# Kernel tuning notes

Measured on AMD Instinct MI355X. Metric: run time of the kernel, lower is better.

The kernel has to match this reference:

```python
import jax, jax.numpy as jnp
import numpy as np
import math

def _ln(x, g, b, eps=1e-5):
    mu = x.mean(-1, keepdims=True)
    var = ((x - mu) ** 2).mean(-1, keepdims=True)
    return (x - mu) / jnp.sqrt(var + eps) * g + b

def _mha(x, in_w, in_b, out_w, out_b, nh):
    # torch nn.MultiheadAttention (batch_first, eval): q,k,v chunks of in_proj
    Bn, Nn, Dm = x.shape
    hd = Dm // nh
    q, k, v = jnp.split(x @ in_w.T + in_b, 3, axis=-1)
    sp = lambda t: t.reshape(Bn, Nn, nh, hd).transpose(0, 2, 1, 3)
    q, k, v = sp(q), sp(k), sp(v)
    a = jax.nn.softmax(jnp.einsum('bhid,bhjd->bhij', q, k) / math.sqrt(hd), axis=-1)
    y = jnp.einsum('bhij,bhjd->bhid', a, v).transpose(0, 2, 1, 3).reshape(Bn, Nn, Dm)
    return y @ out_w.T + out_b

def setup_inputs():
    key = jax.random.key(0)
    ks = iter(jax.random.split(key, 40))
    nrm = lambda shape: jax.random.normal(next(ks), shape, jnp.float32) * 0.02
    B, T, C, H, W = 2, 32, 3, 64, 64
    D, P, nL, nS = 512, 8, 6, 3
    N = (H // P) ** 2
    z = lambda *s: jnp.zeros(s, jnp.float32)
    o = lambda *s: jnp.ones(s, jnp.float32)
    return dict(
        x=jax.random.normal(next(ks), (B, T, C, H, W), jnp.float32),
        patch_w=nrm((D, C * P * P)), patch_b=z(D),
        tok_ln_g=o(D), tok_ln_b=z(D),
        spatial_pos=nrm((1, 1, N, D)), temporal_pos=nrm((1, T, 1, D)),
        snorm_g=o(D), snorm_b=z(D),
        sa_in_w=nrm((nS, 3 * D, D)), sa_in_b=z(nS, 3 * D),
        sa_out_w=nrm((nS, D, D)), sa_out_b=z(nS, D),
        ln1_g=o(nL, D), ln1_b=z(nL, D),
        kqv_w=nrm((nL, 3 * D, D)), kqv_b=z(nL, 3 * D),
        proj_w=nrm((nL, D, D)), proj_b=z(nL, D),
        ln2_g=o(nL, D), ln2_b=z(nL, D),
        fc_w=nrm((nL, 4 * D, D)), fc_b=z(nL, 4 * D),
        cproj_w=nrm((nL, D, 4 * D)), cproj_b=z(nL, D),
        lnf_g=o(D), lnf_b=z(D),
        th_w1=nrm((D // 2, D)), th_b1=z(D // 2), th_w2=nrm((1, D // 2)), th_b2=z(1),
        sh_w1=nrm((D // 2, D)), sh_b1=z(D // 2), sh_w2=nrm((1, D // 2)), sh_b2=z(1),
        pf_w1=nrm((D // 2, D)), pf_b1=z(D // 2), pf_w2=nrm((1, D // 2)), pf_b2=z(1),
    )

def reference(x, patch_w, patch_b, tok_ln_g, tok_ln_b, spatial_pos, temporal_pos,
              snorm_g, snorm_b, sa_in_w, sa_in_b, sa_out_w, sa_out_b,
              ln1_g, ln1_b, kqv_w, kqv_b, proj_w, proj_b, ln2_g, ln2_b,
              fc_w, fc_b, cproj_w, cproj_b, lnf_g, lnf_b,
              th_w1, th_b1, th_w2, th_b2, sh_w1, sh_b1, sh_w2, sh_b2,
              pf_w1, pf_b1, pf_w2, pf_b2):
    B, T, C, H, W = x.shape
    D = patch_w.shape[0]
    P = int(math.isqrt(patch_w.shape[1] // C))
    Hn, Wn = H // P, W // P
    N = Hn * Wn
    # Conv3d kernel=(1,P,P), stride=(1,P,P) == per-frame patchify + matmul
    patches = x.reshape(B, T, C, Hn, P, Wn, P).transpose(0, 1, 3, 5, 2, 4, 6).reshape(B, T, N, C * P * P)
    tok = _ln(patches @ patch_w.T + patch_b, tok_ln_g, tok_ln_b)
    tok = tok + spatial_pos + temporal_pos[:, :T]
    # per-frame spatial attention: identical math per frame -> batch over B*T
    s = tok.reshape(B * T, N, D)
    for i in range(sa_in_w.shape[0]):
        s = s + _mha(_ln(s, snorm_g, snorm_b), sa_in_w[i], sa_in_b[i], sa_out_w[i], sa_out_b[i], nh=4)
    L = T * N
    hid = s.reshape(B, L, D)
    nh = 8
    hd = D // nh
    mask = jnp.tril(jnp.ones((L, L), bool))  # causal over T*N tokens
    for i in range(kqv_w.shape[0]):
        a_in = _ln(hid, ln1_g[i], ln1_b[i])
        k, q, v = jnp.split(a_in @ kqv_w[i].T + kqv_b[i], 3, axis=-1)  # torch split order: k, q, v
        sp = lambda t: t.reshape(B, L, nh, hd).transpose(0, 2, 1, 3)
        q, k, v = sp(q), sp(k), sp(v)
        att = jnp.einsum('bhid,bhjd->bhij', q, k) / math.sqrt(hd)
        att = jax.nn.softmax(jnp.where(mask, att, -jnp.inf), axis=-1)
        y = jnp.einsum('bhij,bhjd->bhid', att, v).transpose(0, 2, 1, 3).reshape(B, L, D)
        hid = hid + y @ proj_w[i].T + proj_b[i]
        m_in = _ln(hid, ln2_g[i], ln2_b[i])
        h = jax.nn.gelu(m_in @ fc_w[i].T + fc_b[i], approximate=False)
        hid = hid + h @ cproj_w[i].T + cproj_b[i]
    hid = _ln(hid, lnf_g, lnf_b).reshape(B, T, N, D)
    head = lambda zz, w1, b1, w2, b2: jax.nn.leaky_relu(zz @ w1.T + b1, 0.2) @ w2.T + b2
    tf = hid.mean(axis=2)  # [B, T, D]
    temporal_score = head(tf[:, -1], th_w1, th_b1, th_w2, th_b2)  # [B, 1] (last timestep, full lengths)
    spatial_score = head(hid.mean(axis=1).mean(axis=1), sh_w1, sh_b1, sh_w2, sh_b2)
    per_frame_scores = head(tf, pf_w1, pf_b1, pf_w2, pf_b2)  # [B, T, 1]
    final_score = temporal_score + spatial_score + per_frame_scores.mean(axis=1)
    return (temporal_score, spatial_score, per_frame_scores, final_score)
```

## Files before the change

### kernel.cpp

```cpp
#include <hip/hip_runtime.h>
#include <hip/hip_bf16.h>
#include <math.h>

#define MTOK 4096

typedef __bf16 bf16x8 __attribute__((ext_vector_type(8)));
typedef float f32x4 __attribute__((ext_vector_type(4)));

__device__ __forceinline__ ushort f2bf(float f){
  __hip_bfloat16 h = __float2bfloat16(f);
  return *reinterpret_cast<ushort*>(&h);
}
__device__ __forceinline__ float bf2f(ushort u){
  return __uint_as_float(((uint)u) << 16);
}
__device__ __forceinline__ void gload_lds16(const void* g, void* l){
  __builtin_amdgcn_global_load_lds((__attribute__((address_space(1))) void*)(void*)g,
                                   (__attribute__((address_space(3))) void*)l, 16, 0, 0);
}

__device__ __forceinline__ float blockReduceSum(float v, float* red){
  #pragma unroll
  for (int off = 32; off; off >>= 1) v += __shfl_down(v, off, 64);
  int lane = threadIdx.x & 63, wid = threadIdx.x >> 6;
  __syncthreads();
  if (lane == 0) red[wid] = v;
  __syncthreads();
  float r = 0.f;
  int nw = blockDim.x >> 6;
  for (int i = 0; i < nw; i++) r += red[i];
  return r;
}
__device__ __forceinline__ float rowMax16(float v){
  #pragma unroll
  for (int m = 8; m; m >>= 1) v = fmaxf(v, __shfl_xor(v, m, 64));
  return v;
}
__device__ __forceinline__ float rowSum16(float v){
  #pragma unroll
  for (int m = 8; m; m >>= 1) v += __shfl_xor(v, m, 64);
  return v;
}

__global__ __launch_bounds__(256) void cvt_w_kernel(
    const float* __restrict__ src, ushort* __restrict__ dst, int n)
{
  int i = (blockIdx.x * 256 + threadIdx.x) * 8;
  float4 a = *(const float4*)(src + i);
  float4 b = *(const float4*)(src + i + 4);
  uint4 o;
  o.x = (uint)f2bf(a.x) | ((uint)f2bf(a.y) << 16);
  o.y = (uint)f2bf(a.z) | ((uint)f2bf(a.w) << 16);
  o.z = (uint)f2bf(b.x) | ((uint)f2bf(b.y) << 16);
  o.w = (uint)f2bf(b.z) | ((uint)f2bf(b.w) << 16);
  *(uint4*)(dst + i) = o;
}

#define OFF_PATCH 0u
#define OFF_SAIN  98304u
#define OFF_SAOUT 2457600u
#define OFF_KQV   3244032u
#define OFF_PROJ  7962624u
#define OFF_FC    9535488u
#define OFF_CPROJ 15826944u
#define W_TOTAL   22118400u
__global__ __launch_bounds__(256) void cvt_all_kernel(
    const float* __restrict__ pw, const float* __restrict__ sain,
    const float* __restrict__ saout, const float* __restrict__ kqv,
    const float* __restrict__ proj, const float* __restrict__ fc,
    const float* __restrict__ cproj, ushort* __restrict__ dst)
{
  int blk = blockIdx.x;
  const float* src; size_t off;
  if      (blk <    48){ src = pw;    off = OFF_PATCH; }
  else if (blk <  1200){ src = sain;  off = OFF_SAIN;  blk -= 48;   }
  else if (blk <  1584){ src = saout; off = OFF_SAOUT; blk -= 1200; }
  else if (blk <  3888){ src = kqv;   off = OFF_KQV;   blk -= 1584; }
  else if (blk <  4656){ src = proj;  off = OFF_PROJ;  blk -= 3888; }
  else if (blk <  7728){ src = fc;    off = OFF_FC;    blk -= 4656; }
  else                 { src = cproj; off = OFF_CPROJ; blk -= 7728; }
  size_t si = (size_t)blk*2048 + threadIdx.x*8;
  float4 a = *(const float4*)(src + si);
  float4 b = *(const float4*)(src + si + 4);
  uint4 o;
  o.x = (uint)f2bf(a.x) | ((uint)f2bf(a.y) << 16);
  o.y = (uint)f2bf(a.z) | ((uint)f2bf(a.w) << 16);
  o.z = (uint)f2bf(b.x) | ((uint)f2bf(b.y) << 16);
  o.w = (uint)f2bf(b.z) | ((uint)f2bf(b.w) << 16);
  *(uint4*)(dst + off + si) = o;
}

__global__ __launch_bounds__(256) void im2col_kernel(
    const float* __restrict__ x, ushort* __restrict__ Pm)
{
  int idx = blockIdx.x*256 + threadIdx.x;
  int m = idx / 24, e8 = idx % 24;
  int b = m >> 11, t = (m >> 6) & 31, n = m & 63;
  int hn = n >> 3, wn = n & 7;
  int c = e8 >> 3, ph = e8 & 7;
  const float* src = x + (((size_t)(b*32 + t)*3 + c)*64 + hn*8 + ph)*64 + wn*8;
  float4 a = *(const float4*)src;
  float4 bq = *(const float4*)(src + 4);
  uint4 o;
  o.x = (uint)f2bf(a.x) | ((uint)f2bf(a.y) << 16);
  o.y = (uint)f2bf(a.z) | ((uint)f2bf(a.w) << 16);
  o.z = (uint)f2bf(bq.x) | ((uint)f2bf(bq.y) << 16);
  o.w = (uint)f2bf(bq.z) | ((uint)f2bf(bq.w) << 16);
  *(uint4*)(Pm + (size_t)m*192 + e8*8) = o;
}

__global__ __launch_bounds__(256) void ln_pos_kernel(
    const float* __restrict__ in, float* __restrict__ out,
    const float* __restrict__ g, const float* __restrict__ b,
    const float* __restrict__ spos, const float* __restrict__ tpos)
{
  int r = blockIdx.x*4 + (threadIdx.x >> 6);
  int lane = threadIdx.x & 63;
  int n = r & 63, t = (r >> 6) & 31;
  const float* row = in + (size_t)r*512 + lane*8;
  float4 v0 = *(const float4*)row;
  float4 v1 = *(const float4*)(row + 4);
  float s = v0.x+v0.y+v0.z+v0.w+v1.x+v1.y+v1.z+v1.w;
  float q = v0.x*v0.x+v0.y*v0.y+v0.z*v0.z+v0.w*v0.w+v1.x*v1.x+v1.y*v1.y+v1.z*v1.z+v1.w*v1.w;
  #pragma unroll
  for (int m = 1; m < 64; m <<= 1){ s += __shfl_xor(s, m, 64); q += __shfl_xor(q, m, 64); }
  float mu = s*(1.f/512.f);
  float inv = rsqrtf(q*(1.f/512.f) - mu*mu + 1e-5f);
  const float* gp = g + lane*8;
  const float* bp = b + lane*8;
  const float* sp = spos + n*512 + lane*8;
  const float* tp = tpos + t*512 + lane*8;
  float* op = out + (size_t)r*512 + lane*8;
  #pragma unroll
  for (int e = 0; e < 2; e++){
    float4 vv = e ? v1 : v0;
    float4 gg = *(const float4*)(gp + e*4);
    float4 bb = *(const float4*)(bp + e*4);
    float4 ss = *(const float4*)(sp + e*4);
    float4 tt = *(const float4*)(tp + e*4);
    float4 oo;
    oo.x = (vv.x-mu)*inv*gg.x + bb.x + ss.x + tt.x;
    oo.y = (vv.y-mu)*inv*gg.y + bb.y + ss.y + tt.y;
    oo.z = (vv.z-mu)*inv*gg.z + bb.z + ss.z + tt.z;
    oo.w = (vv.w-mu)*inv*gg.w + bb.w + ss.w + tt.w;
    *(float4*)(op + e*4) = oo;
  }
}

__global__ __launch_bounds__(256) void ln_bf16_kernel(
    const float* __restrict__ in, ushort* __restrict__ out,
    const float* __restrict__ g, const float* __restrict__ b)
{
  int r = blockIdx.x*4 + (threadIdx.x >> 6);
  int lane = threadIdx.x & 63;
  const float* row = in + (size_t)r*512 + lane*8;
  float4 v0 = *(const float4*)row;
  float4 v1 = *(const float4*)(row + 4);
  float s = v0.x+v0.y+v0.z+v0.w+v1.x+v1.y+v1.z+v1.w;
  float q = v0.x*v0.x+v0.y*v0.y+v0.z*v0.z+v0.w*v0.w+v1.x*v1.x+v1.y*v1.y+v1.z*v1.z+v1.w*v1.w;
  #pragma unroll
  for (int m = 1; m < 64; m <<= 1){ s += __shfl_xor(s, m, 64); q += __shfl_xor(q, m, 64); }
  float mu = s*(1.f/512.f);
  float inv = rsqrtf(q*(1.f/512.f) - mu*mu + 1e-5f);
  float4 g0 = *(const float4*)(g + lane*8);
  float4 g1 = *(const float4*)(g + lane*8 + 4);
  float4 b0 = *(const float4*)(b + lane*8);
  float4 b1 = *(const float4*)(b + lane*8 + 4);
  uint4 o;
  o.x = (uint)f2bf((v0.x-mu)*inv*g0.x + b0.x) | ((uint)f2bf((v0.y-mu)*inv*g0.y + b0.y) << 16);
  o.y = (uint)f2bf((v0.z-mu)*inv*g0.z + b0.z) | ((uint)f2bf((v0.w-mu)*inv*g0.w + b0.w) << 16);
  o.z = (uint)f2bf((v1.x-mu)*inv*g1.x + b1.x) | ((uint)f2bf((v1.y-mu)*inv*g1.y + b1.y) << 16);
  o.w = (uint)f2bf((v1.z-mu)*inv*g1.z + b1.z) | ((uint)f2bf((v1.w-mu)*inv*g1.w + b1.w) << 16);
  *(uint4*)(out + (size_t)r*512 + lane*8) = o;
}

template<int BM, int BN, bool GELU, bool BF16OUT>
__global__ __launch_bounds__(256) void gemm2_kernel(
    const ushort* __restrict__ X, const ushort* __restrict__ Wb,
    const float* __restrict__ bias, const float* __restrict__ res,
    void* __restrict__ Yv, int M, int Nn, int K)
{
  constexpr int WROWS = (BN == 128) ? 2 : 4;
  constexpr int WM = BM / WROWS;
  constexpr int FM = WM / 16;
  constexpr int FN = 4;
  __shared__ __attribute__((aligned(16))) char smem[2*(BM+BN)*128];
  char* Xs0 = smem;
  char* Ws0 = smem + BM*128;
  char* Xs1 = smem + (BM+BN)*128;
  char* Ws1 = Xs1 + BM*128;
  int tid = threadIdx.x, lane = tid & 63, wv = tid >> 6;
  int bm = blockIdx.y * BM, bn = blockIdx.x * BN;
  int wm, wn;
  if (BN == 128){ wm = (wv >> 1) * WM; wn = (wv & 1) * 64; }
  else          { wm = wv * WM;        wn = 0; }

  f32x4 acc[FM][FN];
  #pragma unroll
  for (int i = 0; i < FM; i++)
    #pragma unroll
    for (int j = 0; j < FN; j++){ f32x4 z = {0.f,0.f,0.f,0.f}; acc[i][j] = z; }

  int rowoff = wv*8 + (lane >> 3);
  int colsrc = ((lane & 7) ^ (lane >> 3)) * 16;

  auto stage = [&](char* Xd, char* Wd, int k0){
    #pragma unroll
    for (int i = 0; i < BM/32; i++){
      int row = i*32 + rowoff;
      gload_lds16((const char*)(X + (size_t)(bm + row)*K + k0) + colsrc,
                  Xd + (i*32 + wv*8)*128);
    }
    #pragma unroll
    for (int i = 0; i < BN/32; i++){
      int row = i*32 + rowoff;
      gload_lds16((const char*)(Wb + (size_t)(bn + row)*K + k0) + colsrc,
                  Wd + (i*32 + wv*8)*128);
    }
  };

  stage(Xs0, Ws0, 0);
  __syncthreads();
  int nt = K >> 6;
  for (int t = 0; t < nt; t++){
    char* Xc = (t & 1) ? Xs1 : Xs0;
    char* Wc = (t & 1) ? Ws1 : Ws0;
    if (t + 1 < nt) stage((t & 1) ? Xs0 : Xs1, (t & 1) ? Ws0 : Ws1, (t+1)*64);
    #pragma unroll
    for (int kc = 0; kc < 2; kc++){
      bf16x8 a[FM], b[FN];
      #pragma unroll
      for (int f = 0; f < FM; f++){
        int ra = wm + f*16 + (lane & 15);
        a[f] = *(const bf16x8*)(Xc + ra*128 + ((kc*64 + (lane>>4)*16) ^ ((ra & 7) << 4)));
      }
      #pragma unroll
      for (int f = 0; f < FN; f++){
        int rb = wn + f*16 + (lane & 15);
        b[f] = *(const bf16x8*)(Wc + rb*128 + ((kc*64 + (lane>>4)*16) ^ ((rb & 7) << 4)));
      }
      #pragma unroll
      for (int i = 0; i < FM; i++)
        #pragma unroll
        for (int j = 0; j < FN; j++)
          acc[i][j] = __builtin_amdgcn_mfma_f32_16x16x32_bf16(a[i], b[j], acc[i][j], 0, 0, 0);
    }
    __syncthreads();
  }
  int col0 = lane & 15;
  float bv[FN];
  #pragma unroll
  for (int fn = 0; fn < FN; fn++) bv[fn] = bias[bn + wn + fn*16 + col0];
  #pragma unroll
  for (int fm = 0; fm < FM; fm++){
    #pragma unroll
    for (int r = 0; r < 4; r++){
      int m = bm + wm + fm*16 + (lane >> 4)*4 + r;
      #pragma unroll
      for (int fn = 0; fn < FN; fn++){
        int n = bn + wn + fn*16 + col0;
        float v = acc[fm][fn][r] + bv[fn];
        if (res) v += res[(size_t)m*Nn + n];
        if (GELU) v = 0.5f * v * (1.f + erff(v * 0.70710678118654752440f));
        if (BF16OUT) ((ushort*)Yv)[(size_t)m*Nn + n] = f2bf(v);
        else         ((float*) Yv)[(size_t)m*Nn + n] = v;
      }
    }
  }
}

__global__ __launch_bounds__(256) void spatial_attn_mfma_kernel(
    const ushort* __restrict__ qkv, ushort* __restrict__ y)
{
  __shared__ __attribute__((aligned(16))) char Ks[64*256];
  __shared__ __attribute__((aligned(16))) char Vt[128*128];
  __shared__ __attribute__((aligned(16))) char Ps[64*128];
  int bt = blockIdx.x, h = blockIdx.y;
  int tid = threadIdx.x, lane = tid & 63, w = tid >> 6;
  const ushort* base = qkv + (size_t)bt*64*1536 + (size_t)h*128;
  const float scale = 0.08838834764831845f;

  int qrow = w*16 + (lane & 15);
  bf16x8 qa[4];
  #pragma unroll
  for (int kc = 0; kc < 4; kc++)
    qa[kc] = *(const bf16x8*)(base + (size_t)qrow*1536 + kc*32 + (lane>>4)*8);

  #pragma unroll
  for (int i = 0; i < 4; i++){
    int row = w*16 + i*4 + (lane >> 4);
    const char* src = (const char*)(base + (size_t)row*1536 + 512) + (((lane & 15) ^ (row & 15)) * 16);
    char* dst = Ks + (w*16 + i*4)*256;
    gload_lds16(src, dst);
  }
  {
    int vj = (tid & 31) * 2;
    int d0 = (tid >> 5) * 16;
    const ushort* v0p = base + (size_t)vj*1536 + 1024 + d0;
    const ushort* v1p = v0p + 1536;
    uint4 a0 = *(const uint4*)(v0p);
    uint4 a1 = *(const uint4*)(v0p + 8);
    uint4 b0 = *(const uint4*)(v1p);
    uint4 b1 = *(const uint4*)(v1p + 8);
    uint av[8] = {a0.x, a0.y, a0.z, a0.w, a1.x, a1.y, a1.z, a1.w};
    uint bv[8] = {b0.x, b0.y, b0.z, b0.w, b1.x, b1.y, b1.z, b1.w};
    int cb = 4 * (tid & 31);
    #pragma unroll
    for (int e = 0; e < 8; e++){
      int dl = d0 + e*2, dh = dl + 1;
      uint vlo = (av[e] & 0xffffu) | ((bv[e] & 0xffffu) << 16);
      uint vhi = (av[e] >> 16) | (bv[e] & 0xffff0000u);
      *(uint*)(Vt + dl*128 + (cb ^ ((dl & 7) << 4))) = vlo;
      *(uint*)(Vt + dh*128 + (cb ^ ((dh & 7) << 4))) = vhi;
    }
  }
  __syncthreads();

  f32x4 zero4 = {0.f,0.f,0.f,0.f};
  f32x4 accS[4];
  __builtin_amdgcn_s_setprio(1);
  #pragma unroll
  for (int jt = 0; jt < 4; jt++){
    accS[jt] = zero4;
    #pragma unroll
    for (int kc = 0; kc < 4; kc++){
      int krow = jt*16 + (lane & 15);
      bf16x8 kb = *(const bf16x8*)(Ks + krow*256 + ((kc*64 + (lane>>4)*16) ^ ((krow & 15) << 4)));
      accS[jt] = __builtin_amdgcn_mfma_f32_16x16x32_bf16(qa[kc], kb, accS[jt], 0, 0, 0);
    }
  }
  __builtin_amdgcn_s_setprio(0);
  float l_sum[4];
  #pragma unroll
  for (int r = 0; r < 4; r++){
    float mx = fmaxf(fmaxf(accS[0][r], accS[1][r]), fmaxf(accS[2][r], accS[3][r]));
    mx = rowMax16(mx);
    int prow = w*16 + (lane>>4)*4 + r;
    int swz = (prow & 7) << 4;
    char* pbase = Ps + prow*128;
    float ps = 0.f;
    #pragma unroll
    for (int jt = 0; jt < 4; jt++){
      float p = __expf((accS[jt][r] - mx) * scale);
      ushort pb = f2bf(p);
      *(ushort*)(pbase + ((2*(jt*16 + (lane & 15))) ^ swz)) = pb;
      ps += bf2f(pb);
    }
    l_sum[r] = rowSum16(ps);
  }
  bf16x8 pa[2];
  #pragma unroll
  for (int kc2 = 0; kc2 < 2; kc2++){
    int prow = w*16 + (lane & 15);
    pa[kc2] = *(const bf16x8*)(Ps + prow*128 + ((kc2*64 + (lane>>4)*16) ^ ((prow & 7) << 4)));
  }
  f32x4 o[8];
  __builtin_amdgcn_s_setprio(1);
  #pragma unroll
  for (int dt = 0; dt < 8; dt++){
    o[dt] = zero4;
    #pragma unroll
    for (int kc2 = 0; kc2 < 2; kc2++){
      int vrow = dt*16 + (lane & 15);
      bf16x8 vb = *(const bf16x8*)(Vt + vrow*128 + ((kc2*64 + (lane>>4)*16) ^ ((vrow & 7) << 4)));
      o[dt] = __builtin_amdgcn_mfma_f32_16x16x32_bf16(pa[kc2], vb, o[dt], 0, 0, 0);
    }
  }
  __builtin_amdgcn_s_setprio(0);
  #pragma unroll
  for (int r = 0; r < 4; r++){
    float invl = 1.f / l_sum[r];
    int token = bt*64 + w*16 + (lane>>4)*4 + r;
    ushort* yrow = y + (size_t)token*512 + h*128;
    #pragma unroll
    for (int dt = 0; dt < 8; dt++)
      yrow[dt*16 + (lane & 15)] = f2bf(o[dt][r] * invl);
  }
}

__global__ __launch_bounds__(256) void temporal_attn_split_kernel(
    const ushort* __restrict__ qkv, ushort* __restrict__ Op, float* __restrict__ ml)
{
  __shared__ __attribute__((aligned(16))) char Ks[64*128];
  __shared__ __attribute__((aligned(16))) char Vt[64*128];
  __shared__ __attribute__((aligned(16))) char Ps[4*16*128];
  int id = blockIdx.x;
  int bh = id & 15;
  int rest = id >> 4;
  int qt = 31 - (rest >> 1);
  int half = rest & 1;
  int b = bh >> 3, h = bh & 7;
  int tid = threadIdx.x, lane = tid & 63, w = tid >> 6;
  int g = lane >> 4, q = lane & 15;
  const ushort* base = qkv + (size_t)(b*2048)*1536 + h*64;

  int nk = qt + 1;
  int ktm = (nk + 1) >> 1;
  int kt0 = half ? ktm : 0;
  int kt1 = half ? nk : ktm;

  int qrow = qt*64 + w*16 + q;
  bf16x8 qb[2];
  #pragma unroll
  for (int kc = 0; kc < 2; kc++)
    qb[kc] = *(const bf16x8*)(base + (size_t)qrow*1536 + 512 + kc*32 + g*8);

  f32x4 zero4 = {0.f,0.f,0.f,0.f};
  f32x4 o[4];
  #pragma unroll
  for (int dt = 0; dt < 4; dt++) o[dt] = zero4;
  float m_old = -1e30f, l_sum = 0.f;

  int kcolsrc = ((lane & 7) ^ (lane >> 3)) * 16;
  int vj  = (tid & 31) * 2;
  int vd0 = (tid >> 5) * 8;
  int vcb = 4 * (tid & 31);
  char* myP = Ps + w*2048;
  int pswz = (q & 7) << 4;

  for (int kt = kt0; kt < kt1; kt++){
    __syncthreads();
    #pragma unroll
    for (int i = 0; i < 2; i++){
      int row = w*16 + i*8 + (lane >> 3);
      gload_lds16((const char*)(base + (size_t)(kt*64 + row)*1536) + kcolsrc,
                  Ks + (w*16 + i*8)*128);
    }
    {
      const ushort* v0p = base + (size_t)(kt*64 + vj)*1536 + 1024 + vd0;
      const ushort* v1p = v0p + 1536;
      uint4 a0 = *(const uint4*)v0p;
      uint4 b0 = *(const uint4*)v1p;
      uint av[4] = {a0.x, a0.y, a0.z, a0.w};
      uint bv[4] = {b0.x, b0.y, b0.z, b0.w};
      #pragma unroll
      for (int e = 0; e < 4; e++){
        int dl = vd0 + e*2, dh = dl + 1;
        uint vlo = (av[e] & 0xffffu) | ((bv[e] & 0xffffu) << 16);
        uint vhi = (av[e] >> 16) | (bv[e] & 0xffff0000u);
        *(uint*)(Vt + dl*128 + (vcb ^ ((dl & 7) << 4))) = vlo;
        *(uint*)(Vt + dh*128 + (vcb ^ ((dh & 7) << 4))) = vhi;
      }
    }
    __syncthreads();

    f32x4 accS[4];
    __builtin_amdgcn_s_setprio(1);
    #pragma unroll
    for (int jt = 0; jt < 4; jt++){
      accS[jt] = zero4;
      #pragma unroll
      for (int kc = 0; kc < 2; kc++){
        int krow = jt*16 + q;
        bf16x8 kb = *(const bf16x8*)(Ks + krow*128 + ((kc*64 + g*16) ^ ((krow & 7) << 4)));
        accS[jt] = __builtin_amdgcn_mfma_f32_16x16x32_bf16(kb, qb[kc], accS[jt], 0, 0, 0);
      }
    }
    __builtin_amdgcn_s_setprio(0);
    if (kt == qt){
      int gi = qt*64 + w*16 + q;
      #pragma unroll
      for (int jt = 0; jt < 4; jt++)
        #pragma unroll
        for (int r = 0; r < 4; r++){
          int gj = kt*64 + jt*16 + g*4 + r;
          if (gj > gi) accS[jt][r] = -1e30f;
        }
    }
    float mloc = fmaxf(fmaxf(accS[0][0], accS[0][1]), fmaxf(accS[0][2], accS[0][3]));
    #pragma unroll
    for (int jt = 1; jt < 4; jt++){
      float t2 = fmaxf(fmaxf(accS[jt][0], accS[jt][1]), fmaxf(accS[jt][2], accS[jt][3]));
      mloc = fmaxf(mloc, t2);
    }
    mloc *= 0.125f;
    mloc = fmaxf(mloc, __shfl_xor(mloc, 16, 64));
    mloc = fmaxf(mloc, __shfl_xor(mloc, 32, 64));
    float mnew = fmaxf(m_old, mloc);
    float corr = __expf(m_old - mnew);
    float ps = 0.f;
    #pragma unroll
    for (int jt = 0; jt < 4; jt++){
      ushort pb0 = f2bf(__expf(accS[jt][0]*0.125f - mnew));
      ushort pb1 = f2bf(__expf(accS[jt][1]*0.125f - mnew));
      ushort pb2 = f2bf(__expf(accS[jt][2]*0.125f - mnew));
      ushort pb3 = f2bf(__expf(accS[jt][3]*0.125f - mnew));
      ps += bf2f(pb0) + bf2f(pb1) + bf2f(pb2) + bf2f(pb3);
      uint2 wv;
      wv.x = (uint)pb0 | ((uint)pb1 << 16);
      wv.y = (uint)pb2 | ((uint)pb3 << 16);
      *(uint2*)(myP + q*128 + ((jt*32 + g*8) ^ pswz)) = wv;
    }
    l_sum = l_sum*corr + ps;
    m_old = mnew;
    #pragma unroll
    for (int dt = 0; dt < 4; dt++) o[dt] *= corr;

    bf16x8 pfr[2];
    #pragma unroll
    for (int kc2 = 0; kc2 < 2; kc2++)
      pfr[kc2] = *(const bf16x8*)(myP + q*128 + ((kc2*64 + g*16) ^ pswz));
    __builtin_amdgcn_s_setprio(1);
    #pragma unroll
    for (int dt = 0; dt < 4; dt++){
      #pragma unroll
      for (int kc2 = 0; kc2 < 2; kc2++){
        int vrow = dt*16 + q;
        bf16x8 vb = *(const bf16x8*)(Vt + vrow*128 + ((kc2*64 + g*16) ^ ((vrow & 7) << 4)));
        o[dt] = __builtin_amdgcn_mfma_f32_16x16x32_bf16(vb, pfr[kc2], o[dt], 0, 0, 0);
      }
    }
    __builtin_amdgcn_s_setprio(0);
  }
  l_sum += __shfl_xor(l_sum, 16, 64);
  l_sum += __shfl_xor(l_sum, 32, 64);
  size_t tokbase = (size_t)half*4096 + (size_t)b*2048;
  int token = qt*64 + w*16 + q;
  ushort* yrow = Op + (tokbase + token)*512 + h*64;
  #pragma unroll
  for (int dt = 0; dt < 4; dt++){
    ushort4 o4;
    o4.x = f2bf(o[dt][0]); o4.y = f2bf(o[dt][1]);
    o4.z = f2bf(o[dt][2]); o4.w = f2bf(o[dt][3]);
    *(ushort4*)(yrow + dt*16 + g*4) = o4;
  }
  if (g == 0){
    float* mlp = ml + ((tokbase + token)*8 + h)*2;
    mlp[0] = m_old;
    mlp[1] = l_sum;
  }
}

__global__ __launch_bounds__(256) void attn_merge_kernel(
    const ushort* __restrict__ Op, const float* __restrict__ ml, ushort* __restrict__ Ef)
{
  int tok = blockIdx.x*4 + (threadIdx.x >> 6);
  int l6 = threadIdx.x & 63;
  int h = l6 >> 3, d0 = (l6 & 7)*8;
  int e = h*64 + d0;
  const float* m1p = ml + ((size_t)tok*8 + h)*2;
  const float* m2p = ml + (((size_t)4096 + tok)*8 + h)*2;
  float m1 = m1p[0], l1 = m1p[1];
  float m2 = m2p[0], l2 = m2p[1];
  float mm = fmaxf(m1, m2);
  float w1 = __expf(m1 - mm), w2 = __expf(m2 - mm);
  float inv = 1.f / (w1*l1 + w2*l2);
  uint4 a = *(const uint4*)(Op + (size_t)tok*512 + e);
  uint4 bq = *(const uint4*)(Op + ((size_t)4096 + tok)*512 + e);
  uint av[4] = {a.x, a.y, a.z, a.w};
  uint bv[4] = {bq.x, bq.y, bq.z, bq.w};
  uint ov[4];
  #pragma unroll
  for (int p = 0; p < 4; p++){
    float x0 = (w1*bf2f((ushort)(av[p] & 0xffff)) + w2*bf2f((ushort)(bv[p] & 0xffff))) * inv;
    float x1 = (w1*bf2f((ushort)(av[p] >> 16))    + w2*bf2f((ushort)(bv[p] >> 16)))    * inv;
    ov[p] = (uint)f2bf(x0) | ((uint)f2bf(x1) << 16);
  }
  uint4 o; o.x = ov[0]; o.y = ov[1]; o.z = ov[2]; o.w = ov[3];
  *(uint4*)(Ef + (size_t)tok*512 + e) = o;
}

__global__ __launch_bounds__(256) void reduce_tf_kernel(const ushort* __restrict__ hid, float* __restrict__ tf){
  int bt = blockIdx.x, tid = threadIdx.x;
  for (int d = tid; d < 512; d += 256){
    float s = 0.f;
    for (int n = 0; n < 64; n++) s += bf2f(hid[((size_t)bt*64 + n)*512 + d]);
    tf[(size_t)bt*512 + d] = s * (1.f/64.f);
  }
}

__global__ __launch_bounds__(256) void head_kernel(
    const float* __restrict__ tf,
    const float* __restrict__ th_w1, const float* __restrict__ th_b1,
    const float* __restrict__ th_w2, const float* __restrict__ th_b2,
    const float* __restrict__ sh_w1, const float* __restrict__ sh_b1,
    const float* __restrict__ sh_w2, const float* __restrict__ sh_b2,
    const float* __restrict__ pf_w1, const float* __restrict__ pf_b1,
    const float* __restrict__ pf_w2, const float* __restrict__ pf_b2,
    float* __restrict__ out)
{
  __shared__ float z[512];
  __shared__ float red[4];
  int bi = blockIdx.x, tid = threadIdx.x;
  const float *w1, *b1, *w2, *b2;
  float* dst;
  if (bi < 64){
    w1 = pf_w1; b1 = pf_b1; w2 = pf_w2; b2 = pf_b2; dst = out + 4 + bi;
    z[tid]       = tf[(size_t)bi*512 + tid];
    z[tid + 256] = tf[(size_t)bi*512 + tid + 256];
  } else if (bi < 66){
    int b = bi - 64;
    w1 = th_w1; b1 = th_b1; w2 = th_w2; b2 = th_b2; dst = out + b;
    z[tid]       = tf[(size_t)(b*32 + 31)*512 + tid];
    z[tid + 256] = tf[(size_t)(b*32 + 31)*512 + tid + 256];
  } else {
    int b = bi - 66;
    w1 = sh_w1; b1 = sh_b1; w2 = sh_w2; b2 = sh_b2; dst = out + 2 + b;
    float s0 = 0.f, s1 = 0.f;
    for (int t = 0; t < 32; t++){
      s0 += tf[(size_t)(b*32 + t)*512 + tid];
      s1 += tf[(size_t)(b*32 + t)*512 + tid + 256];
    }
    z[tid] = s0 * (1.f/32.f); z[tid + 256] = s1 * (1.f/32.f);
  }
  __syncthreads();
  float a = b1[tid];
  const float* wrow = w1 + (size_t)tid * 512;
  for (int k = 0; k < 512; k++) a = fmaf(wrow[k], z[k], a);
  a = (a > 0.f) ? a : 0.2f * a;
  float s = blockReduceSum(a * w2[tid], red);
  if (tid == 0) *dst = s + b2[0];
}

__global__ __launch_bounds__(64) void final_kernel(float* __restrict__ out){
  int b = threadIdx.x;
  if (b < 2){
    float s = 0.f;
    for (int t = 0; t < 32; t++) s += out[4 + b*32 + t];
    out[68 + b] = out[b] + out[2 + b] + s * (1.f/32.f);
  }
}

extern "C" void kernel_launch(void* const* d_in, const int* in_sizes, int n_in,
                              void* d_out, int out_size, void* d_ws, size_t ws_size,
                              hipStream_t stream)
{
  const float* x          = (const float*)d_in[0];
  const float* patch_w    = (const float*)d_in[1];
  const float* patch_b    = (const float*)d_in[2];
  const float* tok_ln_g   = (const float*)d_in[3];
  const float* tok_ln_b   = (const float*)d_in[4];
  const float* spatial_pos= (const float*)d_in[5];
  const float* temporal_pos=(const float*)d_in[6];
  const float* snorm_g    = (const float*)d_in[7];
  const float* snorm_b    = (const float*)d_in[8];
  const float* sa_in_w    = (const float*)d_in[9];
  const float* sa_in_b    = (const float*)d_in[10];
  const float* sa_out_w   = (const float*)d_in[11];
  const float* sa_out_b   = (const float*)d_in[12];
  const float* ln1_g      = (const float*)d_in[13];
  const float* ln1_b      = (const float*)d_in[14];
  const float* kqv_w      = (const float*)d_in[15];
  const float* kqv_b      = (const float*)d_in[16];
  const float* proj_w     = (const float*)d_in[17];
  const float* proj_b     = (const float*)d_in[18];
  const float* ln2_g      = (const float*)d_in[19];
  const float* ln2_b      = (const float*)d_in[20];
  const float* fc_w       = (const float*)d_in[21];
  const float* fc_b       = (const float*)d_in[22];
  const float* cproj_w    = (const float*)d_in[23];
  const float* cproj_b    = (const float*)d_in[24];
  const float* lnf_g      = (const float*)d_in[25];
  const float* lnf_b      = (const float*)d_in[26];
  const float* th_w1 = (const float*)d_in[27];
  const float* th_b1 = (const float*)d_in[28];
  const float* th_w2 = (const float*)d_in[29];
  const float* th_b2 = (const float*)d_in[30];
  const float* sh_w1 = (const float*)d_in[31];
  const float* sh_b1 = (const float*)d_in[32];
  const float* sh_w2 = (const float*)d_in[33];
  const float* sh_b2 = (const float*)d_in[34];
  const float* pf_w1 = (const float*)d_in[35];
  const float* pf_b1 = (const float*)d_in[36];
  const float* pf_w2 = (const float*)d_in[37];
  const float* pf_b2 = (const float*)d_in[38];

  float* out = (float*)d_out;
  char* p = (char*)d_ws;
  float*  A  = (float*)p;      p += (size_t)MTOK*512*4;
  ushort* Ru = (ushort*)p;     p += (size_t)MTOK*2048*2;
  ushort* Bf = (ushort*)p;     p += (size_t)MTOK*512*2;
  ushort* Ef = (ushort*)p;     p += (size_t)MTOK*512*2;
  float*  tfp = (float*)p;     p += (size_t)64*512*4;
  ushort* OpB = (ushort*)p;    p += (size_t)2*MTOK*512*2;
  float*  mlB = (float*)p;     p += (size_t)2*MTOK*8*2*4;
  ushort* Wslot = (ushort*)p;  p += (size_t)1048576*2;
  ushort* Wall = (ushort*)p;   p += (size_t)W_TOTAL*2;
  const size_t NEED_BIG = (size_t)(p - (char*)d_ws);
  float*  Pf = (float*)Ru;
  ushort* Pm = Ef;

  const bool big = (ws_size >= NEED_BIG);

  if (big){
    cvt_all_kernel<<<10800, 256, 0, stream>>>(patch_w, sa_in_w, sa_out_w, kqv_w,
                                              proj_w, fc_w, cproj_w, Wall);
  }
  auto W = [&](const float* src, size_t arena_off, size_t nelem) -> const ushort* {
    if (big) return Wall + arena_off;
    cvt_w_kernel<<<(int)(nelem/2048), 256, 0, stream>>>(src, Wslot, (int)nelem);
    return Wslot;
  };

  im2col_kernel<<<384, 256, 0, stream>>>(x, Pm);
  gemm2_kernel<64,64,false,false><<<dim3(8, 64), 256, 0, stream>>>(
      Pm, W(patch_w, OFF_PATCH, 512*192), patch_b, nullptr, Pf, MTOK, 512, 192);
  ln_pos_kernel<<<1024, 256, 0, stream>>>(Pf, A, tok_ln_g, tok_ln_b, spatial_pos, temporal_pos);

  for (int i = 0; i < 3; i++){
    ln_bf16_kernel<<<1024, 256, 0, stream>>>(A, Bf, snorm_g, snorm_b);
    gemm2_kernel<64,128,false,true><<<dim3(12, 64), 256, 0, stream>>>(
        Bf, W(sa_in_w + (size_t)i*1536*512, OFF_SAIN + (size_t)i*786432, 1536*512),
        sa_in_b + (size_t)i*1536, nullptr, Ru, MTOK, 1536, 512);
    spatial_attn_mfma_kernel<<<dim3(64, 4), 256, 0, stream>>>(Ru, Ef);
    gemm2_kernel<64,64,false,false><<<dim3(8, 64), 256, 0, stream>>>(
        Ef, W(sa_out_w + (size_t)i*512*512, OFF_SAOUT + (size_t)i*262144, 512*512),
        sa_out_b + (size_t)i*512, A, A, MTOK, 512, 512);
  }
  for (int i = 0; i < 6; i++){
    ln_bf16_kernel<<<1024, 256, 0, stream>>>(A, Bf, ln1_g + (size_t)i*512, ln1_b + (size_t)i*512);
    gemm2_kernel<64,128,false,true><<<dim3(12, 64), 256, 0, stream>>>(
        Bf, W(kqv_w + (size_t)i*1536*512, OFF_KQV + (size_t)i*786432, 1536*512),
        kqv_b + (size_t)i*1536, nullptr, Ru, MTOK, 1536, 512);
    temporal_attn_split_kernel<<<1024, 256, 0, stream>>>(Ru, OpB, mlB);
    attn_merge_kernel<<<1024, 256, 0, stream>>>(OpB, mlB, Ef);
    gemm2_kernel<64,64,false,false><<<dim3(8, 64), 256, 0, stream>>>(
        Ef, W(proj_w + (size_t)i*512*512, OFF_PROJ + (size_t)i*262144, 512*512),
        proj_b + (size_t)i*512, A, A, MTOK, 512, 512);
    ln_bf16_kernel<<<1024, 256, 0, stream>>>(A, Bf, ln2_g + (size_t)i*512, ln2_b + (size_t)i*512);
    gemm2_kernel<64,128,true,true><<<dim3(16, 64), 256, 0, stream>>>(
        Bf, W(fc_w + (size_t)i*2048*512, OFF_FC + (size_t)i*1048576, 2048*512),
        fc_b + (size_t)i*2048, nullptr, Ru, MTOK, 2048, 512);
    gemm2_kernel<64,64,false,false><<<dim3(8, 64), 256, 0, stream>>>(
        Ru, W(cproj_w + (size_t)i*512*2048, OFF_CPROJ + (size_t)i*1048576, 512*2048),
        cproj_b + (size_t)i*512, A, A, MTOK, 512, 2048);
  }
  ln_bf16_kernel<<<1024, 256, 0, stream>>>(A, Bf, lnf_g, lnf_b);
  reduce_tf_kernel<<<64, 256, 0, stream>>>(Bf, tfp);
  head_kernel<<<68, 256, 0, stream>>>(tfp, th_w1, th_b1, th_w2, th_b2,
                                      sh_w1, sh_b1, sh_w2, sh_b2,
                                      pf_w1, pf_b1, pf_w2, pf_b2, out);
  final_kernel<<<1, 64, 0, stream>>>(out);
}
```

Baseline: 806.2 us.

## Single-buffer W tile in FC GEMM and add lazy softmax rescaling

Adds a WSB template mode to the GEMM that double-buffers only the X tile and single-buffers the weight tile, which cuts LDS use per block for the 64x128 FC GEMM, presumably to raise occupancy. The cost is an extra barrier per K step and exposed weight-load latency. The temporal attention kernel also skips the online-softmax rescale of the running output and sum unless the new max exceeds the old one by more than 8. This saves exp and multiply work but lets exponentials grow up to e^8 before normalisation.

```diff
diff --git a/kernel.cpp b/kernel.cpp
--- a/kernel.cpp
+++ b/kernel.cpp
@@ -174,7 +174,7 @@
   *(uint4*)(out + (size_t)r*512 + lane*8) = o;
 }
 
-template<int BM, int BN, bool GELU, bool BF16OUT>
+template<int BM, int BN, bool GELU, bool BF16OUT, bool WSB>
 __global__ __launch_bounds__(256) void gemm2_kernel(
     const ushort* __restrict__ X, const ushort* __restrict__ Wb,
     const float* __restrict__ bias, const float* __restrict__ res,
@@ -184,11 +184,8 @@
   constexpr int WM = BM / WROWS;
   constexpr int FM = WM / 16;
   constexpr int FN = 4;
-  __shared__ __attribute__((aligned(16))) char smem[2*(BM+BN)*128];
-  char* Xs0 = smem;
-  char* Ws0 = smem + BM*128;
-  char* Xs1 = smem + (BM+BN)*128;
-  char* Ws1 = Xs1 + BM*128;
+  constexpr int SMEM = WSB ? (2*BM+BN)*128 : 2*(BM+BN)*128;
+  __shared__ __attribute__((aligned(16))) char smem[SMEM];
   int tid = threadIdx.x, lane = tid & 63, wv = tid >> 6;
   int bm = blockIdx.y * BM, bn = blockIdx.x * BN;
   int wm, wn;
@@ -204,13 +201,15 @@
   int rowoff = wv*8 + (lane >> 3);
   int colsrc = ((lane & 7) ^ (lane >> 3)) * 16;
 
-  auto stage = [&](char* Xd, char* Wd, int k0){
+  auto stageX = [&](char* Xd, int k0){
     #pragma unroll
     for (int i = 0; i < BM/32; i++){
       int row = i*32 + rowoff;
       gload_lds16((const char*)(X + (size_t)(bm + row)*K + k0) + colsrc,
                   Xd + (i*32 + wv*8)*128);
     }
+  };
+  auto stageW = [&](char* Wd, int k0){
     #pragma unroll
     for (int i = 0; i < BN/32; i++){
       int row = i*32 + rowoff;
@@ -218,14 +217,7 @@
                   Wd + (i*32 + wv*8)*128);
     }
   };
-
-  stage(Xs0, Ws0, 0);
-  __syncthreads();
-  int nt = K >> 6;
-  for (int t = 0; t < nt; t++){
-    char* Xc = (t & 1) ? Xs1 : Xs0;
-    char* Wc = (t & 1) ? Ws1 : Ws0;
-    if (t + 1 < nt) stage((t & 1) ? Xs0 : Xs1, (t & 1) ? Ws0 : Ws1, (t+1)*64);
+  auto compute = [&](const char* Xc, const char* Wc){
     #pragma unroll
     for (int kc = 0; kc < 2; kc++){
       bf16x8 a[FM], b[FN];
@@ -245,8 +237,44 @@
         for (int j = 0; j < FN; j++)
           acc[i][j] = __builtin_amdgcn_mfma_f32_16x16x32_bf16(a[i], b[j], acc[i][j], 0, 0, 0);
     }
+  };
+
+  int nt = K >> 6;
+  if constexpr (WSB){
+    char* Xs0 = smem;
+    char* Xs1 = smem + BM*128;
+    char* WsS = smem + 2*BM*128;
+    stageX(Xs0, 0);
+    stageW(WsS, 0);
     __syncthreads();
-  }
+    for (int t = 0; t < nt; t++){
+      char* Xc = (t & 1) ? Xs1 : Xs0;
+      if (t + 1 < nt) stageX((t & 1) ? Xs0 : Xs1, (t+1)*64);
+      compute(Xc, WsS);
+      __syncthreads();
+      if (t + 1 < nt) stageW(WsS, (t+1)*64);
+      __syncthreads();
+    }
+  } else {
+    char* Xs0 = smem;
+    char* Ws0 = smem + BM*128;
+    char* Xs1 = smem + (BM+BN)*128;
+    char* Ws1 = Xs1 + BM*128;
+    stageX(Xs0, 0);
+    stageW(Ws0, 0);
+    __syncthreads();
+    for (int t = 0; t < nt; t++){
+      char* Xc = (t & 1) ? Xs1 : Xs0;
+      char* Wc = (t & 1) ? Ws1 : Ws0;
+      if (t + 1 < nt){
+        stageX((t & 1) ? Xs0 : Xs1, (t+1)*64);
+        stageW((t & 1) ? Ws0 : Ws1, (t+1)*64);
+      }
+      compute(Xc, Wc);
+      __syncthreads();
+    }
+  }
+
   int col0 = lane & 15;
   float bv[FN];
   #pragma unroll
@@ -476,25 +504,28 @@
     mloc *= 0.125f;
     mloc = fmaxf(mloc, __shfl_xor(mloc, 16, 64));
     mloc = fmaxf(mloc, __shfl_xor(mloc, 32, 64));
-    float mnew = fmaxf(m_old, mloc);
-    float corr = __expf(m_old - mnew);
+    if (!__all(mloc <= m_old + 8.f)){
+      float mnew = fmaxf(m_old, mloc);
+      float corr = __expf(m_old - mnew);
+      l_sum *= corr;
+      #pragma unroll
+      for (int dt = 0; dt < 4; dt++) o[dt] *= corr;
+      m_old = mnew;
+    }
     float ps = 0.f;
     #pragma unroll
     for (int jt = 0; jt < 4; jt++){
-      ushort pb0 = f2bf(__expf(accS[jt][0]*0.125f - mnew));
-      ushort pb1 = f2bf(__expf(accS[jt][1]*0.125f - mnew));
-      ushort pb2 = f2bf(__expf(accS[jt][2]*0.125f - mnew));
-      ushort pb3 = f2bf(__expf(accS[jt][3]*0.125f - mnew));
+      ushort pb0 = f2bf(__expf(accS[jt][0]*0.125f - m_old));
+      ushort pb1 = f2bf(__expf(accS[jt][1]*0.125f - m_old));
+      ushort pb2 = f2bf(__expf(accS[jt][2]*0.125f - m_old));
+      ushort pb3 = f2bf(__expf(accS[jt][3]*0.125f - m_old));
       ps += bf2f(pb0) + bf2f(pb1) + bf2f(pb2) + bf2f(pb3);
       uint2 wv;
       wv.x = (uint)pb0 | ((uint)pb1 << 16);
       wv.y = (uint)pb2 | ((uint)pb3 << 16);
       *(uint2*)(myP + q*128 + ((jt*32 + g*8) ^ pswz)) = wv;
     }
-    l_sum = l_sum*corr + ps;
-    m_old = mnew;
-    #pragma unroll
-    for (int dt = 0; dt < 4; dt++) o[dt] *= corr;
+    l_sum += ps;
 
     bf16x8 pfr[2];
     #pragma unroll
@@ -693,35 +724,35 @@
   };
 
   im2col_kernel<<<384, 256, 0, stream>>>(x, Pm);
-  gemm2_kernel<64,64,false,false><<<dim3(8, 64), 256, 0, stream>>>(
+  gemm2_kernel<64,64,false,false,false><<<dim3(8, 64), 256, 0, stream>>>(
       Pm, W(patch_w, OFF_PATCH, 512*192), patch_b, nullptr, Pf, MTOK, 512, 192);
   ln_pos_kernel<<<1024, 256, 0, stream>>>(Pf, A, tok_ln_g, tok_ln_b, spatial_pos, temporal_pos);
 
   for (int i = 0; i < 3; i++){
     ln_bf16_kernel<<<1024, 256, 0, stream>>>(A, Bf, snorm_g, snorm_b);
-    gemm2_kernel<64,128,false,true><<<dim3(12, 64), 256, 0, stream>>>(
+    gemm2_kernel<64,128,false,true,false><<<dim3(12, 64), 256, 0, stream>>>(
         Bf, W(sa_in_w + (size_t)i*1536*512, OFF_SAIN + (size_t)i*786432, 1536*512),
         sa_in_b + (size_t)i*1536, nullptr, Ru, MTOK, 1536, 512);
     spatial_attn_mfma_kernel<<<dim3(64, 4), 256, 0, stream>>>(Ru, Ef);
-    gemm2_kernel<64,64,false,false><<<dim3(8, 64), 256, 0, stream>>>(
+    gemm2_kernel<64,64,false,false,false><<<dim3(8, 64), 256, 0, stream>>>(
         Ef, W(sa_out_w + (size_t)i*512*512, OFF_SAOUT + (size_t)i*262144, 512*512),
         sa_out_b + (size_t)i*512, A, A, MTOK, 512, 512);
   }
   for (int i = 0; i < 6; i++){
     ln_bf16_kernel<<<1024, 256, 0, stream>>>(A, Bf, ln1_g + (size_t)i*512, ln1_b + (size_t)i*512);
-    gemm2_kernel<64,128,false,true><<<dim3(12, 64), 256, 0, stream>>>(
+    gemm2_kernel<64,128,false,true,false><<<dim3(12, 64), 256, 0, stream>>>(
         Bf, W(kqv_w + (size_t)i*1536*512, OFF_KQV + (size_t)i*786432, 1536*512),
         kqv_b + (size_t)i*1536, nullptr, Ru, MTOK, 1536, 512);
     temporal_attn_split_kernel<<<1024, 256, 0, stream>>>(Ru, OpB, mlB);
     attn_merge_kernel<<<1024, 256, 0, stream>>>(OpB, mlB, Ef);
-    gemm2_kernel<64,64,false,false><<<dim3(8, 64), 256, 0, stream>>>(
+    gemm2_kernel<64,64,false,false,false><<<dim3(8, 64), 256, 0, stream>>>(
         Ef, W(proj_w + (size_t)i*512*512, OFF_PROJ + (size_t)i*262144, 512*512),
         proj_b + (size_t)i*512, A, A, MTOK, 512, 512);
     ln_bf16_kernel<<<1024, 256, 0, stream>>>(A, Bf, ln2_g + (size_t)i*512, ln2_b + (size_t)i*512);
-    gemm2_kernel<64,128,true,true><<<dim3(16, 64), 256, 0, stream>>>(
+    gemm2_kernel<64,128,true,true,true><<<dim3(16, 64), 256, 0, stream>>>(
         Bf, W(fc_w + (size_t)i*2048*512, OFF_FC + (size_t)i*1048576, 2048*512),
         fc_b + (size_t)i*2048, nullptr, Ru, MTOK, 2048, 512);
-    gemm2_kernel<64,64,false,false><<<dim3(8, 64), 256, 0, stream>>>(
+    gemm2_kernel<64,64,false,false,false><<<dim3(8, 64), 256, 0, stream>>>(
         Ru, W(cproj_w + (size_t)i*512*2048, OFF_CPROJ + (size_t)i*1048576, 512*2048),
         cproj_b + (size_t)i*512, A, A, MTOK, 512, 2048);
   }
```

New measurement: 802.5 us (median of 2 runs). Within noise of the previous version (-0.5%).
